# Kernel optimization log

Hardware: AMD Instinct MI355X
Metric: run time of the kernel (lower is better)

Reference implementation:

```python
import jax, jax.numpy as jnp
import numpy as np

NUM_LOW, NUM_HIGH, DIM = 8192, 1024, 2048
EPS = 1e-10


def sparsemax(z):
    # z: [..., K]; Martins & Astudillo sparsemax along last axis.
    K = z.shape[-1]
    z_sorted = jnp.flip(jnp.sort(z, axis=-1), axis=-1)          # descending
    z_cum = jnp.cumsum(z_sorted, axis=-1)
    k = jnp.arange(1, K + 1, dtype=z.dtype)
    support = (1.0 + k * z_sorted) > z_cum                       # bool [..., K]
    k_sup = jnp.sum(support, axis=-1, keepdims=True)             # int [..., 1]
    tau = (jnp.take_along_axis(z_cum, k_sup - 1, axis=-1) - 1.0) / k_sup.astype(z.dtype)
    return jnp.maximum(z - tau, 0.0)


def normalize_rows(x, eps=EPS):
    return x / (jnp.sum(x, axis=1, keepdims=True) + eps)


def setup_inputs() -> dict:
    key = jax.random.key(0)
    k1, k2, k3, k4 = jax.random.split(key, 4)

    def xavier(k, shape):
        bound = float(np.sqrt(6.0 / (shape[0] + shape[1])))
        return jax.random.uniform(k, shape, jnp.float32, -bound, bound)

    return {
        "low_w": xavier(k1, (NUM_LOW, DIM)),    # low Concepts parameter
        "high_w": xavier(k2, (NUM_HIGH, DIM)),  # high Concepts parameter
        "Wq": xavier(k3, (DIM, DIM)),           # q_linear.weight (keep_head_dim, n_head=1)
        "Wk": xavier(k4, (DIM, DIM)),           # k_linear.weight
        "norm_low_concepts": 1,
        "norm_high_concepts": 1,
    }


def reference(low_w, high_w, Wq, Wk, norm_low_concepts, norm_high_concepts):
    # Concepts modules: return (possibly normalized) concepts + cosine similarity.
    low_normed = low_w / jnp.linalg.norm(low_w, axis=1, keepdims=True)
    low_concepts = low_normed if norm_low_concepts else low_w
    low_cos = low_normed @ low_normed.T                          # [NL, NL]

    high_normed = high_w / jnp.linalg.norm(high_w, axis=1, keepdims=True)
    high_concepts = high_normed if norm_high_concepts else high_w
    high_cos = high_normed @ high_normed.T                       # [NH, NH]

    # detach_low_concepts=True -> queries do not receive gradients
    low_q = jax.lax.stop_gradient(low_concepts)

    # ModifiedMultiHeadAttention (n_head=1, keep_head_dim -> d_head=DIM; eval mode,
    # so smooth_max is identity and sparsemax is deterministic).
    q = low_q @ Wq.T                                             # [NL, D]
    k = high_concepts @ Wk.T                                     # [NH, D]
    scale = 1.0 / jnp.sqrt(jnp.asarray(DIM, q.dtype))
    attn = sparsemax((q @ k.T) * scale)                          # [NL, NH]
    high_related_low = attn @ high_concepts                      # [NL, D]

    # output_high_concepts_type == "high_plus_low": add back aggregated low concepts
    aggregated_low = normalize_rows(attn.T) @ low_q              # [NH, D]
    output_high_concepts = high_related_low + attn @ aggregated_low  # [NL, D]

    return (low_concepts, low_cos, output_high_concepts, high_cos, attn)
```

## Files before the change

### kernel.cpp

```cpp
#include <hip/hip_runtime.h>
#include <hip/hip_bf16.h>
#include <stdint.h>

#define NL   8192
#define NHI  1024
#define DIMV 2048

typedef __attribute__((ext_vector_type(8))) short short8;
typedef __attribute__((ext_vector_type(4))) float f32x4;

__device__ __forceinline__ unsigned short f2bf(float x){
  unsigned u = __float_as_uint(x);
  u += 0x7FFFu + ((u >> 16) & 1u);
  return (unsigned short)(u >> 16);
}
__device__ __forceinline__ float bf2f(unsigned short b){
  return __uint_as_float(((unsigned)b) << 16);
}
__device__ __forceinline__ unsigned pack2bf(float a, float b){
  return (unsigned)f2bf(a) | ((unsigned)f2bf(b) << 16);
}

__device__ __forceinline__ void gload16(const void* g, void* l){
  __builtin_amdgcn_global_load_lds(
      (const __attribute__((address_space(1))) unsigned int*)g,
      (__attribute__((address_space(3))) unsigned int*)l, 16, 0, 0);
}

template<int WRITE_F32>
__global__ __launch_bounds__(256)
void rownorm_kernel(const float* __restrict__ W, float* __restrict__ outF32,
                    unsigned short* __restrict__ outBf){
  int row = blockIdx.x;
  const float* r = W + (size_t)row * DIMV;
  int base = threadIdx.x * 8;
  float4 x0 = *(const float4*)(r + base);
  float4 x1 = *(const float4*)(r + base + 4);
  float ss = x0.x*x0.x + x0.y*x0.y + x0.z*x0.z + x0.w*x0.w
           + x1.x*x1.x + x1.y*x1.y + x1.z*x1.z + x1.w*x1.w;
  #pragma unroll
  for(int s = 1; s < 64; s <<= 1) ss += __shfl_xor(ss, s, 64);
  __shared__ float red[4];
  if((threadIdx.x & 63) == 0) red[threadIdx.x >> 6] = ss;
  __syncthreads();
  float tot = red[0] + red[1] + red[2] + red[3];
  float inv = 1.0f / sqrtf(tot);
  float y0=x0.x*inv, y1=x0.y*inv, y2=x0.z*inv, y3=x0.w*inv;
  float y4=x1.x*inv, y5=x1.y*inv, y6=x1.z*inv, y7=x1.w*inv;
  if(WRITE_F32){
    float* o = outF32 + (size_t)row * DIMV + base;
    *(float4*)o       = make_float4(y0,y1,y2,y3);
    *(float4*)(o + 4) = make_float4(y4,y5,y6,y7);
  }
  uint4 u;
  u.x = pack2bf(y0,y1); u.y = pack2bf(y2,y3);
  u.z = pack2bf(y4,y5); u.w = pack2bf(y6,y7);
  *(uint4*)(outBf + (size_t)row * DIMV + base) = u;
}

__global__ __launch_bounds__(256)
void cast_bf16_kernel(const float* __restrict__ in, unsigned short* __restrict__ out){
  size_t i = ((size_t)blockIdx.x * 256 + threadIdx.x) * 8;
  float4 x0 = *(const float4*)(in + i);
  float4 x1 = *(const float4*)(in + i + 4);
  uint4 u;
  u.x = pack2bf(x0.x,x0.y); u.y = pack2bf(x0.z,x0.w);
  u.z = pack2bf(x1.x,x1.y); u.w = pack2bf(x1.z,x1.w);
  *(uint4*)(out + i) = u;
}

template<int OUT_BF16, int MIRROR>
__global__ __launch_bounds__(256, 2)
void gemm_bt_kernel(const unsigned short* __restrict__ A,
                    const unsigned short* __restrict__ Bt,
                    float* __restrict__ Cf, unsigned short* __restrict__ Cb,
                    int M, int N, int K, float scale){
  __shared__ __align__(16) char smem[32768];
  unsigned short* sA = (unsigned short*)smem;
  unsigned short* sB = sA + 128 * 64;

  int tid = threadIdx.x, lane = tid & 63, wid = tid >> 6;
  int mBase, nBase;
  if(MIRROR){
    int nwg = gridDim.x;
    int id = blockIdx.x;
    int cpx = nwg >> 3;
    id = (id & 7) * cpx + (id >> 3);
    int bi = 0;
    while(((bi+1)*64 - (((bi+1)*bi) >> 1)) <= id) bi++;
    int off = bi*64 - ((bi*(bi-1)) >> 1);
    int bj = bi + (id - off);
    mBase = bi * 128; nBase = bj * 128;
  } else {
    int gx = gridDim.x, gy = gridDim.y;
    int nwg = gx * gy;
    int id = blockIdx.y * gx + blockIdx.x;
    if((nwg & 7) == 0){ int cpx = nwg >> 3; id = (id & 7) * cpx + (id >> 3); }
    mBase = (id / gx) * 128; nBase = (id % gx) * 128;
  }

  int chRow = lane >> 3;
  int chCol = (lane & 7) * 8;
  int wm = wid >> 1, wn = wid & 1;

  f32x4 acc[4][4];
  #pragma unroll
  for(int i=0;i<4;i++)
    #pragma unroll
    for(int j=0;j<4;j++) acc[i][j] = (f32x4){0.f,0.f,0.f,0.f};

  int kChunk = K / (int)gridDim.z;
  int kStart = kChunk * (int)blockIdx.z;
  if(!OUT_BF16) Cf += (size_t)blockIdx.z * M * N;

  for(int k0 = kStart; k0 < kStart + kChunk; k0 += 64){
    #pragma unroll
    for(int i = 0; i < 4; i++){
      int ch = wid * 4 + i;
      int arow = ch * 8 + chRow;
      gload16(A  + (size_t)(mBase + arow) * K + k0 + chCol, &sA[ch * 512]);
      gload16(Bt + (size_t)(nBase + arow) * K + k0 + chCol, &sB[ch * 512]);
    }
    __syncthreads();
    #pragma unroll
    for(int kk = 0; kk < 64; kk += 32){
      short8 a[4], b[4];
      int krd = kk + (lane >> 4) * 8;
      #pragma unroll
      for(int i = 0; i < 4; i++){
        int row = wm * 64 + i * 16 + (lane & 15);
        a[i] = *reinterpret_cast<const short8*>(&sA[row * 64 + krd]);
        int col = wn * 64 + i * 16 + (lane & 15);
        b[i] = *reinterpret_cast<const short8*>(&sB[col * 64 + krd]);
      }
      #pragma unroll
      for(int i = 0; i < 4; i++)
        #pragma unroll
        for(int j = 0; j < 4; j++)
          acc[i][j] = __builtin_amdgcn_mfma_f32_16x16x32_bf16(a[i], b[j], acc[i][j], 0, 0, 0);
    }
    __syncthreads();
  }

  #pragma unroll
  for(int i = 0; i < 4; i++){
    #pragma unroll
    for(int j = 0; j < 4; j++){
      int row = mBase + wm * 64 + i * 16 + (lane >> 4) * 4;
      int col = nBase + wn * 64 + j * 16 + (lane & 15);
      #pragma unroll
      for(int r = 0; r < 4; r++){
        float v = acc[i][j][r] * scale;
        size_t off = (size_t)(row + r) * N + col;
        if(OUT_BF16) Cb[off] = f2bf(v);
        else         Cf[off] = v;
      }
    }
  }

  if(MIRROR && mBase != nBase){
    float* tf = (float*)smem;
    #pragma unroll
    for(int rq = 0; rq < 4; rq++){
      int qm = rq >> 1, qn = rq & 1;
      __syncthreads();
      if(wm == qm && wn == qn){
        #pragma unroll
        for(int i = 0; i < 4; i++)
          #pragma unroll
          for(int j = 0; j < 4; j++){
            int rl = i * 16 + (lane >> 4) * 4;
            int cl = j * 16 + (lane & 15);
            #pragma unroll
            for(int r = 0; r < 4; r++)
              tf[(rl + r) * 65 + cl] = acc[i][j][r] * scale;
          }
      }
      __syncthreads();
      int mr = tid >> 2, seg = tid & 3;
      size_t obase = (size_t)(nBase + qn * 64 + mr) * N + mBase + qm * 64 + seg * 16;
      #pragma unroll
      for(int k4 = 0; k4 < 4; k4++){
        float4 v;
        v.x = tf[(seg * 16 + k4 * 4 + 0) * 65 + mr];
        v.y = tf[(seg * 16 + k4 * 4 + 1) * 65 + mr];
        v.z = tf[(seg * 16 + k4 * 4 + 2) * 65 + mr];
        v.w = tf[(seg * 16 + k4 * 4 + 3) * 65 + mr];
        *(float4*)(Cf + obase + k4 * 4) = v;
      }
    }
  }
}

__global__ __launch_bounds__(256)
void sparsemax_kernel(float* __restrict__ S, unsigned short* __restrict__ attnBf){
  int wid = threadIdx.x >> 6, lane = threadIdx.x & 63;
  int row = blockIdx.x * 4 + wid;
  float* z = S + (size_t)row * NHI;
  float v[16];
  #pragma unroll
  for(int j = 0; j < 16; j++) v[j] = z[j * 64 + lane];
  float mx = v[0];
  #pragma unroll
  for(int j = 1; j < 16; j++) mx = fmaxf(mx, v[j]);
  #pragma unroll
  for(int s = 1; s < 64; s <<= 1) mx = fmaxf(mx, __shfl_xor(mx, s, 64));
  float lo = mx - 1.0f, hi = mx;
  for(int it = 0; it < 40; it++){
    float mid = 0.5f * (lo + hi);
    float sum = 0.f;
    #pragma unroll
    for(int j = 0; j < 16; j++) sum += fmaxf(v[j] - mid, 0.f);
    #pragma unroll
    for(int s = 1; s < 64; s <<= 1) sum += __shfl_xor(sum, s, 64);
    if(sum >= 1.0f) lo = mid; else hi = mid;
  }
  float cnt = 0.f, ssum = 0.f;
  #pragma unroll
  for(int j = 0; j < 16; j++){
    if(v[j] > lo){ cnt += 1.f; ssum += v[j]; }
  }
  #pragma unroll
  for(int s = 1; s < 64; s <<= 1){
    cnt  += __shfl_xor(cnt,  s, 64);
    ssum += __shfl_xor(ssum, s, 64);
  }
  float tau = (ssum - 1.0f) / cnt;
  #pragma unroll
  for(int j = 0; j < 16; j++){
    float a = fmaxf(v[j] - tau, 0.f);
    z[j * 64 + lane] = a;
    attnBf[(size_t)row * NHI + j * 64 + lane] = f2bf(a);
  }
}

__global__ __launch_bounds__(256)
void colsum_part_kernel(const float* __restrict__ attn, float* __restrict__ part){
  int chunk = blockIdx.x;
  int t = threadIdx.x;
  const float* p = attn + (size_t)chunk * 32 * NHI;
  float a0=0,a1=0,a2=0,a3=0;
  for(int r = 0; r < 32; r++){
    a0 += p[(size_t)r*NHI + t];
    a1 += p[(size_t)r*NHI + t + 256];
    a2 += p[(size_t)r*NHI + t + 512];
    a3 += p[(size_t)r*NHI + t + 768];
  }
  float* q = part + (size_t)chunk * NHI;
  q[t]=a0; q[t+256]=a1; q[t+512]=a2; q[t+768]=a3;
}
__global__ __launch_bounds__(256)
void colsum_final_kernel(const float* __restrict__ part, float* __restrict__ colsum){
  int c = blockIdx.x * 256 + threadIdx.x;
  float s = 0.f;
  for(int i = 0; i < 256; i++) s += part[(size_t)i * NHI + c];
  colsum[c] = s;
}

__global__ __launch_bounds__(256)
void transpose_bf16_kernel(const unsigned short* __restrict__ in,
                           unsigned short* __restrict__ out, int R, int C){
  __shared__ unsigned short tile[64][65];
  int c0 = blockIdx.x * 64, r0 = blockIdx.y * 64;
  int t = threadIdx.x;
  int ci = t & 63, r4 = t >> 6;
  #pragma unroll
  for(int k = 0; k < 16; k++){
    int r = k * 4 + r4;
    tile[r][ci] = in[(size_t)(r0 + r) * C + c0 + ci];
  }
  __syncthreads();
  #pragma unroll
  for(int k = 0; k < 16; k++){
    int cc = k * 4 + r4;
    out[(size_t)(c0 + cc) * R + r0 + ci] = tile[ci][cc];
  }
}

__global__ __launch_bounds__(256)
void mt_kernel(const unsigned short* __restrict__ highNT, const float* __restrict__ aggP,
               const float* __restrict__ colsum, unsigned short* __restrict__ Mt){
  int idx = blockIdx.x * 256 + threadIdx.x;
  int h = idx & 1023;
  float s = aggP[idx] + aggP[idx + 2097152] + aggP[idx + 4194304] + aggP[idx + 6291456];
  float val = bf2f(highNT[idx]) + s / (colsum[h] + 1e-10f);
  Mt[idx] = f2bf(val);
}

extern "C" void kernel_launch(void* const* d_in, const int* in_sizes, int n_in,
                              void* d_out, int out_size, void* d_ws, size_t ws_size,
                              hipStream_t stream){
  const float* low_w  = (const float*)d_in[0];
  const float* high_w = (const float*)d_in[1];
  const float* Wq     = (const float*)d_in[2];
  const float* Wk     = (const float*)d_in[3];
  float* out = (float*)d_out;

  char* ws = (char*)d_ws;
  unsigned short* lowN  = (unsigned short*)(ws);
  float*          aggP  = (float*)(ws);
  unsigned short* highN = (unsigned short*)(ws + 33554432);
  unsigned short* WqB   = (unsigned short*)(ws + 37748736);
  unsigned short* WkB   = (unsigned short*)(ws + 46137344);
  unsigned short* attnB = (unsigned short*)(ws + 37748736);
  unsigned short* qB    = (unsigned short*)(ws + 54525952);
  unsigned short* lowNT = qB;
  unsigned short* kB    = (unsigned short*)(ws + 88080384);
  float*          part  = (float*)(ws + 88080384);
  float*          colsum= (float*)(ws + 88080384 + 1048576);
  unsigned short* attnT = (unsigned short*)(ws + 92274688);
  unsigned short* Mt    = (unsigned short*)(ws + 109051904);
  unsigned short* highNT= (unsigned short*)(ws + 113246208);

  float* out_lowc    = out;
  float* out_lowcos  = out + 16777216;
  float* out_high    = out + 83886080;
  float* out_highcos = out + 100663296;
  float* out_attn    = out + 101711872;

  const float scl = 1.0f / sqrtf((float)DIMV);

  rownorm_kernel<1><<<NL,  256, 0, stream>>>(low_w,  out_lowc, lowN);
  rownorm_kernel<0><<<NHI, 256, 0, stream>>>(high_w, nullptr,  highN);
  cast_bf16_kernel<<<2048, 256, 0, stream>>>(Wq, WqB);
  cast_bf16_kernel<<<2048, 256, 0, stream>>>(Wk, WkB);
  gemm_bt_kernel<0,1><<<2080, 256, 0, stream>>>(lowN, lowN, out_lowcos, nullptr,
                                                NL, NL, DIMV, 1.0f);
  gemm_bt_kernel<0,0><<<dim3(8,8), 256, 0, stream>>>(highN, highN, out_highcos, nullptr,
                                                     NHI, NHI, DIMV, 1.0f);
  gemm_bt_kernel<1,0><<<dim3(16,64), 256, 0, stream>>>(lowN, WqB, nullptr, qB,
                                                       NL, DIMV, DIMV, 1.0f);
  gemm_bt_kernel<1,0><<<dim3(16,8), 256, 0, stream>>>(highN, WkB, nullptr, kB,
                                                      NHI, DIMV, DIMV, 1.0f);
  gemm_bt_kernel<0,0><<<dim3(8,64), 256, 0, stream>>>(qB, kB, out_attn, nullptr,
                                                      NL, NHI, DIMV, scl);
  sparsemax_kernel<<<NL/4, 256, 0, stream>>>(out_attn, attnB);
  colsum_part_kernel<<<256, 256, 0, stream>>>(out_attn, part);
  colsum_final_kernel<<<4, 256, 0, stream>>>(part, colsum);
  transpose_bf16_kernel<<<dim3(NHI/64, NL/64), 256, 0, stream>>>(attnB, attnT, NL, NHI);
  transpose_bf16_kernel<<<dim3(DIMV/64, NL/64), 256, 0, stream>>>(lowN, lowNT, NL, DIMV);
  transpose_bf16_kernel<<<dim3(DIMV/64, NHI/64), 256, 0, stream>>>(highN, highNT, NHI, DIMV);
  gemm_bt_kernel<0,0><<<dim3(8,16,4), 256, 0, stream>>>(lowNT, attnT, aggP, nullptr,
                                                        DIMV, NHI, NL, 1.0f);
  mt_kernel<<<8192, 256, 0, stream>>>(highNT, aggP, colsum, Mt);
  gemm_bt_kernel<0,0><<<dim3(16,64), 256, 0, stream>>>(attnB, Mt, out_high, nullptr,
                                                       NL, DIMV, NHI, 1.0f);
}
```

Before: 680.8 us.

## Add 256x256-tile 8-wave GEMM with double-buffered async LDS pipeline for large GEMMs

Adds a new GEMM kernel that computes 256x256 output tiles with 512 threads. It double-buffers tiles in LDS through direct global-to-LDS loads with XOR-swizzled columns, and interleaves the next tile's loads with MFMA phases under barriers and raised wave priority. The large GEMMs (low cosine with the mirrored triangle, Q projection, attention scores, final output) move to it, while the smaller ones keep the 128x128 kernel, which loses its mirror path. The larger tiles aim to raise arithmetic intensity and overlap memory with compute. In exchange, the 128KB of LDS limits occupancy, and small grids such as the 128-block score GEMM may underfill the GPU.

```diff
diff --git a/kernel.cpp b/kernel.cpp
--- a/kernel.cpp
+++ b/kernel.cpp
@@ -69,7 +69,167 @@
   *(uint4*)(out + i) = u;
 }
 
+
+__device__ __forceinline__ void stageA2(const unsigned short* __restrict__ G, int ldk,
+                                        int row0, int kt, int scol, char* dst0,
+                                        int tid, int srl){
+  gload16(G + (size_t)(row0 + srl)*ldk + kt*64 + scol, dst0 + tid*16);
+  gload16(G + (size_t)(row0 + 128 + srl)*ldk + kt*64 + scol, dst0 + 16384 + tid*16);
+}
+__device__ __forceinline__ void stageB2(const unsigned short* __restrict__ G, int ldk,
+                                        int row0, int kt, int scol, char* dst0,
+                                        int tid, int srl){
+  gload16(G + (size_t)(row0 + srl)*ldk + kt*64 + scol, dst0 + tid*16);
+  gload16(G + (size_t)(row0 + 64 + srl)*ldk + kt*64 + scol, dst0 + 8192 + tid*16);
+}
+
+#define PHASE(MH, CB, PRE) { \
+  short8 a0_ = *(const short8*)(pa + ((MH)*64 +  0 + rA)*128 + (CB)); \
+  short8 a1_ = *(const short8*)(pa + ((MH)*64 + 16 + rA)*128 + (CB)); \
+  short8 a2_ = *(const short8*)(pa + ((MH)*64 + 32 + rA)*128 + (CB)); \
+  short8 a3_ = *(const short8*)(pa + ((MH)*64 + 48 + rA)*128 + (CB)); \
+  short8 b0_ = *(const short8*)(pb + (rB0 +  0)*128 + (CB)); \
+  short8 b1_ = *(const short8*)(pb + (rB0 + 16)*128 + (CB)); \
+  short8 b2_ = *(const short8*)(pb + (rB0 + 32)*128 + (CB)); \
+  short8 b3_ = *(const short8*)(pb + (rB0 + 48)*128 + (CB)); \
+  PRE; \
+  __builtin_amdgcn_s_barrier(); \
+  asm volatile("s_waitcnt lgkmcnt(0)" ::: "memory"); \
+  __builtin_amdgcn_sched_barrier(0); \
+  __builtin_amdgcn_s_setprio(1); \
+  acc[(MH)*4+0][0] = __builtin_amdgcn_mfma_f32_16x16x32_bf16(a0_, b0_, acc[(MH)*4+0][0],0,0,0); \
+  acc[(MH)*4+0][1] = __builtin_amdgcn_mfma_f32_16x16x32_bf16(a0_, b1_, acc[(MH)*4+0][1],0,0,0); \
+  acc[(MH)*4+0][2] = __builtin_amdgcn_mfma_f32_16x16x32_bf16(a0_, b2_, acc[(MH)*4+0][2],0,0,0); \
+  acc[(MH)*4+0][3] = __builtin_amdgcn_mfma_f32_16x16x32_bf16(a0_, b3_, acc[(MH)*4+0][3],0,0,0); \
+  acc[(MH)*4+1][0] = __builtin_amdgcn_mfma_f32_16x16x32_bf16(a1_, b0_, acc[(MH)*4+1][0],0,0,0); \
+  acc[(MH)*4+1][1] = __builtin_amdgcn_mfma_f32_16x16x32_bf16(a1_, b1_, acc[(MH)*4+1][1],0,0,0); \
+  acc[(MH)*4+1][2] = __builtin_amdgcn_mfma_f32_16x16x32_bf16(a1_, b2_, acc[(MH)*4+1][2],0,0,0); \
+  acc[(MH)*4+1][3] = __builtin_amdgcn_mfma_f32_16x16x32_bf16(a1_, b3_, acc[(MH)*4+1][3],0,0,0); \
+  acc[(MH)*4+2][0] = __builtin_amdgcn_mfma_f32_16x16x32_bf16(a2_, b0_, acc[(MH)*4+2][0],0,0,0); \
+  acc[(MH)*4+2][1] = __builtin_amdgcn_mfma_f32_16x16x32_bf16(a2_, b1_, acc[(MH)*4+2][1],0,0,0); \
+  acc[(MH)*4+2][2] = __builtin_amdgcn_mfma_f32_16x16x32_bf16(a2_, b2_, acc[(MH)*4+2][2],0,0,0); \
+  acc[(MH)*4+2][3] = __builtin_amdgcn_mfma_f32_16x16x32_bf16(a2_, b3_, acc[(MH)*4+2][3],0,0,0); \
+  acc[(MH)*4+3][0] = __builtin_amdgcn_mfma_f32_16x16x32_bf16(a3_, b0_, acc[(MH)*4+3][0],0,0,0); \
+  acc[(MH)*4+3][1] = __builtin_amdgcn_mfma_f32_16x16x32_bf16(a3_, b1_, acc[(MH)*4+3][1],0,0,0); \
+  acc[(MH)*4+3][2] = __builtin_amdgcn_mfma_f32_16x16x32_bf16(a3_, b2_, acc[(MH)*4+3][2],0,0,0); \
+  acc[(MH)*4+3][3] = __builtin_amdgcn_mfma_f32_16x16x32_bf16(a3_, b3_, acc[(MH)*4+3][3],0,0,0); \
+  __builtin_amdgcn_s_setprio(0); \
+  __builtin_amdgcn_s_barrier(); \
+}
+
 template<int OUT_BF16, int MIRROR>
+__global__ __launch_bounds__(512, 2)
+void gemm256_kernel(const unsigned short* __restrict__ A,
+                    const unsigned short* __restrict__ Bt,
+                    float* __restrict__ Cf, unsigned short* __restrict__ Cb,
+                    int M, int N, int K, float scale){
+  __shared__ __align__(16) char smem[131072];
+  int tid = threadIdx.x, lane = tid & 63, wid = tid >> 6;
+  int wm = wid >> 2, wn = wid & 3;
+
+  int mBase, nBase;
+  if(MIRROR){
+    int nwg = gridDim.x;
+    int id = blockIdx.x;
+    int cpx = nwg >> 3;
+    id = (id & 7) * cpx + (id >> 3);
+    int bi = 0;
+    while(((bi+1)*32 - (((bi+1)*bi) >> 1)) <= id) bi++;
+    int off = bi*32 - ((bi*(bi-1)) >> 1);
+    int bj = bi + (id - off);
+    mBase = bi * 256; nBase = bj * 256;
+  } else {
+    int gx = gridDim.x;
+    int nwg = gx * gridDim.y;
+    int id = blockIdx.y * gx + blockIdx.x;
+    if((nwg & 7) == 0){ int cpx = nwg >> 3; id = (id & 7) * cpx + (id >> 3); }
+    mBase = (id / gx) * 256; nBase = (id % gx) * 256;
+  }
+
+  f32x4 acc[8][4];
+  #pragma unroll
+  for(int i=0;i<8;i++)
+    #pragma unroll
+    for(int j=0;j<4;j++) acc[i][j] = (f32x4){0.f,0.f,0.f,0.f};
+
+  int srl  = tid >> 3;
+  int scol = (((tid & 7) * 16) ^ ((srl & 7) << 4)) >> 1;
+  int rA  = lane & 15;
+  int rB0 = (wn & 1) * 64 + rA;
+  int cbK0 = (((lane >> 4) * 16)      ^ ((lane & 7) << 4));
+  int cbK1 = ((64 + (lane >> 4) * 16) ^ ((lane & 7) << 4));
+
+  int nT = K >> 6;
+  stageB2(Bt, K, nBase,       0, scol, smem + 65536,         tid, srl);
+  stageB2(Bt, K, nBase + 128, 0, scol, smem + 65536 + 16384, tid, srl);
+  stageA2(A,  K, mBase,       0, scol, smem,                 tid, srl);
+  stageA2(A,  K, mBase + 64,  0, scol, smem + 8192,          tid, srl);
+  asm volatile("s_waitcnt vmcnt(2)" ::: "memory");
+  __builtin_amdgcn_s_barrier();
+
+  for(int t = 0; t < nT; ++t){
+    int d = t & 1, d1 = d ^ 1, k1 = t + 1;
+    bool st = (k1 < nT);
+    const char* pa = smem + d*32768 + wm*16384;
+    const char* pb = smem + 65536 + d*32768 + (wn>>1)*16384;
+    PHASE(0, cbK0,
+      if(st){ stageB2(Bt, K, nBase, k1, scol, smem + 65536 + d1*32768, tid, srl);
+              asm volatile("s_waitcnt vmcnt(2)" ::: "memory"); }
+      else  { asm volatile("s_waitcnt vmcnt(0)" ::: "memory"); } )
+    PHASE(1, cbK0,
+      if(st) stageB2(Bt, K, nBase + 128, k1, scol, smem + 65536 + d1*32768 + 16384, tid, srl); )
+    PHASE(0, cbK1,
+      if(st) stageA2(A, K, mBase, k1, scol, smem + d1*32768, tid, srl); )
+    PHASE(1, cbK1,
+      if(st){ stageA2(A, K, mBase + 64, k1, scol, smem + d1*32768 + 8192, tid, srl);
+              asm volatile("s_waitcnt vmcnt(2)" ::: "memory"); } )
+  }
+
+  int crow0 = mBase + wm*128 + (lane>>4)*4;
+  int ccol0 = nBase + wn*64 + (lane&15);
+  #pragma unroll
+  for(int i=0;i<8;i++)
+    #pragma unroll
+    for(int j=0;j<4;j++)
+      #pragma unroll
+      for(int r=0;r<4;r++){
+        float v = acc[i][j][r] * scale;
+        size_t off = (size_t)(crow0 + i*16 + r) * N + ccol0 + j*16;
+        if(OUT_BF16) Cb[off] = f2bf(v);
+        else         Cf[off] = v;
+      }
+
+  if(MIRROR && mBase != nBase){
+    float* T = (float*)(void*)(smem + wid * 8448);
+    int ln15 = lane & 15, lh = lane >> 4;
+    #pragma unroll
+    for(int c2 = 0; c2 < 4; c2++){
+      #pragma unroll
+      for(int ii = 0; ii < 2; ii++)
+        #pragma unroll
+        for(int j = 0; j < 4; j++)
+          #pragma unroll
+          for(int r = 0; r < 4; r++)
+            T[(j*16 + ln15)*33 + ii*16 + lh*4 + r] = acc[c2*2+ii][j][r] * scale;
+      asm volatile("s_waitcnt lgkmcnt(0)" ::: "memory");
+      __builtin_amdgcn_sched_barrier(0);
+      size_t gb = (size_t)(nBase + wn*64 + lane) * N + (mBase + wm*128 + c2*32);
+      #pragma unroll
+      for(int k4 = 0; k4 < 8; k4++){
+        float4 v;
+        v.x = T[lane*33 + k4*4 + 0];
+        v.y = T[lane*33 + k4*4 + 1];
+        v.z = T[lane*33 + k4*4 + 2];
+        v.w = T[lane*33 + k4*4 + 3];
+        *(float4*)(Cf + gb + k4*4) = v;
+      }
+      asm volatile("s_waitcnt lgkmcnt(0)" ::: "memory");
+      __builtin_amdgcn_sched_barrier(0);
+    }
+  }
+}
+
+template<int OUT_BF16>
 __global__ __launch_bounds__(256, 2)
 void gemm_bt_kernel(const unsigned short* __restrict__ A,
                     const unsigned short* __restrict__ Bt,
@@ -80,24 +240,11 @@
   unsigned short* sB = sA + 128 * 64;
 
   int tid = threadIdx.x, lane = tid & 63, wid = tid >> 6;
-  int mBase, nBase;
-  if(MIRROR){
-    int nwg = gridDim.x;
-    int id = blockIdx.x;
-    int cpx = nwg >> 3;
-    id = (id & 7) * cpx + (id >> 3);
-    int bi = 0;
-    while(((bi+1)*64 - (((bi+1)*bi) >> 1)) <= id) bi++;
-    int off = bi*64 - ((bi*(bi-1)) >> 1);
-    int bj = bi + (id - off);
-    mBase = bi * 128; nBase = bj * 128;
-  } else {
-    int gx = gridDim.x, gy = gridDim.y;
-    int nwg = gx * gy;
-    int id = blockIdx.y * gx + blockIdx.x;
-    if((nwg & 7) == 0){ int cpx = nwg >> 3; id = (id & 7) * cpx + (id >> 3); }
-    mBase = (id / gx) * 128; nBase = (id % gx) * 128;
-  }
+  int gx = gridDim.x, gy = gridDim.y;
+  int nwg = gx * gy;
+  int id = blockIdx.y * gx + blockIdx.x;
+  if((nwg & 7) == 0){ int cpx = nwg >> 3; id = (id & 7) * cpx + (id >> 3); }
+  int mBase = (id / gx) * 128, nBase = (id % gx) * 128;
 
   int chRow = lane >> 3;
   int chCol = (lane & 7) * 8;
@@ -154,39 +301,6 @@
         size_t off = (size_t)(row + r) * N + col;
         if(OUT_BF16) Cb[off] = f2bf(v);
         else         Cf[off] = v;
-      }
-    }
-  }
-
-  if(MIRROR && mBase != nBase){
-    float* tf = (float*)smem;
-    #pragma unroll
-    for(int rq = 0; rq < 4; rq++){
-      int qm = rq >> 1, qn = rq & 1;
-      __syncthreads();
-      if(wm == qm && wn == qn){
-        #pragma unroll
-        for(int i = 0; i < 4; i++)
-          #pragma unroll
-          for(int j = 0; j < 4; j++){
-            int rl = i * 16 + (lane >> 4) * 4;
-            int cl = j * 16 + (lane & 15);
-            #pragma unroll
-            for(int r = 0; r < 4; r++)
-              tf[(rl + r) * 65 + cl] = acc[i][j][r] * scale;
-          }
-      }
-      __syncthreads();
-      int mr = tid >> 2, seg = tid & 3;
-      size_t obase = (size_t)(nBase + qn * 64 + mr) * N + mBase + qm * 64 + seg * 16;
-      #pragma unroll
-      for(int k4 = 0; k4 < 4; k4++){
-        float4 v;
-        v.x = tf[(seg * 16 + k4 * 4 + 0) * 65 + mr];
-        v.y = tf[(seg * 16 + k4 * 4 + 1) * 65 + mr];
-        v.z = tf[(seg * 16 + k4 * 4 + 2) * 65 + mr];
-        v.w = tf[(seg * 16 + k4 * 4 + 3) * 65 + mr];
-        *(float4*)(Cf + obase + k4 * 4) = v;
       }
     }
   }
@@ -324,15 +438,15 @@
   rownorm_kernel<0><<<NHI, 256, 0, stream>>>(high_w, nullptr,  highN);
   cast_bf16_kernel<<<2048, 256, 0, stream>>>(Wq, WqB);
   cast_bf16_kernel<<<2048, 256, 0, stream>>>(Wk, WkB);
-  gemm_bt_kernel<0,1><<<2080, 256, 0, stream>>>(lowN, lowN, out_lowcos, nullptr,
-                                                NL, NL, DIMV, 1.0f);
-  gemm_bt_kernel<0,0><<<dim3(8,8), 256, 0, stream>>>(highN, highN, out_highcos, nullptr,
-                                                     NHI, NHI, DIMV, 1.0f);
-  gemm_bt_kernel<1,0><<<dim3(16,64), 256, 0, stream>>>(lowN, WqB, nullptr, qB,
-                                                       NL, DIMV, DIMV, 1.0f);
-  gemm_bt_kernel<1,0><<<dim3(16,8), 256, 0, stream>>>(highN, WkB, nullptr, kB,
-                                                      NHI, DIMV, DIMV, 1.0f);
-  gemm_bt_kernel<0,0><<<dim3(8,64), 256, 0, stream>>>(qB, kB, out_attn, nullptr,
+  gemm256_kernel<0,1><<<528, 512, 0, stream>>>(lowN, lowN, out_lowcos, nullptr,
+                                               NL, NL, DIMV, 1.0f);
+  gemm_bt_kernel<0><<<dim3(8,8), 256, 0, stream>>>(highN, highN, out_highcos, nullptr,
+                                                   NHI, NHI, DIMV, 1.0f);
+  gemm256_kernel<1,0><<<dim3(8,32), 512, 0, stream>>>(lowN, WqB, nullptr, qB,
+                                                      NL, DIMV, DIMV, 1.0f);
+  gemm_bt_kernel<1><<<dim3(16,8), 256, 0, stream>>>(highN, WkB, nullptr, kB,
+                                                    NHI, DIMV, DIMV, 1.0f);
+  gemm256_kernel<0,0><<<dim3(4,32), 512, 0, stream>>>(qB, kB, out_attn, nullptr,
                                                       NL, NHI, DIMV, scl);
   sparsemax_kernel<<<NL/4, 256, 0, stream>>>(out_attn, attnB);
   colsum_part_kernel<<<256, 256, 0, stream>>>(out_attn, part);
@@ -340,9 +454,9 @@
   transpose_bf16_kernel<<<dim3(NHI/64, NL/64), 256, 0, stream>>>(attnB, attnT, NL, NHI);
   transpose_bf16_kernel<<<dim3(DIMV/64, NL/64), 256, 0, stream>>>(lowN, lowNT, NL, DIMV);
   transpose_bf16_kernel<<<dim3(DIMV/64, NHI/64), 256, 0, stream>>>(highN, highNT, NHI, DIMV);
-  gemm_bt_kernel<0,0><<<dim3(8,16,4), 256, 0, stream>>>(lowNT, attnT, aggP, nullptr,
-                                                        DIMV, NHI, NL, 1.0f);
+  gemm_bt_kernel<0><<<dim3(8,16,4), 256, 0, stream>>>(lowNT, attnT, aggP, nullptr,
+                                                      DIMV, NHI, NL, 1.0f);
   mt_kernel<<<8192, 256, 0, stream>>>(highNT, aggP, colsum, Mt);
-  gemm_bt_kernel<0,0><<<dim3(16,64), 256, 0, stream>>>(attnB, Mt, out_high, nullptr,
-                                                       NL, DIMV, NHI, 1.0f);
-}
+  gemm256_kernel<0,0><<<dim3(8,32), 512, 0, stream>>>(attnB, Mt, out_high, nullptr,
+                                                      NL, DIMV, NHI, 1.0f);
+}
```

After: 730.2 us. +7.3%, slower.

## Split-K small GEMMs and merge cast and transpose launches

Applied to the files above, without the earlier changes.

The two Wq/Wk casts are merged into one launch, and the three transposes into one kernel with a block-id dispatch. Both are meant to cut launch overhead and the tails of small grids. The high_cos and k-projection GEMMs, which only had 64 and 128 blocks, now use split-K over 2 slices into fp32 scratch plus a combine kernel, to fill more CUs. This adds extra scratch traffic and two small combine launches, and depends on the gemm kernel already handling gridDim.z as a K split and on the scratch regions not overlapping live buffers.

```diff
diff --git a/kernel.cpp b/kernel.cpp
--- a/kernel.cpp
+++ b/kernel.cpp
@@ -59,8 +59,12 @@
 }
 
 __global__ __launch_bounds__(256)
-void cast_bf16_kernel(const float* __restrict__ in, unsigned short* __restrict__ out){
-  size_t i = ((size_t)blockIdx.x * 256 + threadIdx.x) * 8;
+void cast2_kernel(const float* __restrict__ a, const float* __restrict__ b,
+                  unsigned short* __restrict__ oa, unsigned short* __restrict__ ob){
+  int id = blockIdx.x;
+  const float* in; unsigned short* out;
+  if(id < 2048){ in = a; out = oa; } else { in = b; out = ob; id -= 2048; }
+  size_t i = ((size_t)id * 256 + threadIdx.x) * 8;
   float4 x0 = *(const float4*)(in + i);
   float4 x1 = *(const float4*)(in + i + 4);
   uint4 u;
@@ -193,6 +197,31 @@
 }
 
 __global__ __launch_bounds__(256)
+void combine_bf16_kernel(const float* __restrict__ p, unsigned short* __restrict__ out,
+                         size_t stride){
+  size_t i = ((size_t)blockIdx.x * 256 + threadIdx.x) * 8;
+  float4 a0 = *(const float4*)(p + i);
+  float4 a1 = *(const float4*)(p + i + 4);
+  float4 b0 = *(const float4*)(p + stride + i);
+  float4 b1 = *(const float4*)(p + stride + i + 4);
+  uint4 u;
+  u.x = pack2bf(a0.x+b0.x, a0.y+b0.y); u.y = pack2bf(a0.z+b0.z, a0.w+b0.w);
+  u.z = pack2bf(a1.x+b1.x, a1.y+b1.y); u.w = pack2bf(a1.z+b1.z, a1.w+b1.w);
+  *(uint4*)(out + i) = u;
+}
+__global__ __launch_bounds__(256)
+void combine_f32_kernel(const float* __restrict__ p, float* __restrict__ out,
+                        size_t stride){
+  size_t i = ((size_t)blockIdx.x * 256 + threadIdx.x) * 8;
+  float4 a0 = *(const float4*)(p + i);
+  float4 a1 = *(const float4*)(p + i + 4);
+  float4 b0 = *(const float4*)(p + stride + i);
+  float4 b1 = *(const float4*)(p + stride + i + 4);
+  *(float4*)(out + i)     = make_float4(a0.x+b0.x, a0.y+b0.y, a0.z+b0.z, a0.w+b0.w);
+  *(float4*)(out + i + 4) = make_float4(a1.x+b1.x, a1.y+b1.y, a1.z+b1.z, a1.w+b1.w);
+}
+
+__global__ __launch_bounds__(256)
 void sparsemax_kernel(float* __restrict__ S, unsigned short* __restrict__ attnBf){
   int wid = threadIdx.x >> 6, lane = threadIdx.x & 63;
   int row = blockIdx.x * 4 + wid;
@@ -258,10 +287,18 @@
 }
 
 __global__ __launch_bounds__(256)
-void transpose_bf16_kernel(const unsigned short* __restrict__ in,
-                           unsigned short* __restrict__ out, int R, int C){
+void transpose3_kernel(const unsigned short* __restrict__ attnB, unsigned short* __restrict__ attnT,
+                       const unsigned short* __restrict__ lowN,  unsigned short* __restrict__ lowNT,
+                       const unsigned short* __restrict__ highN, unsigned short* __restrict__ highNT){
   __shared__ unsigned short tile[64][65];
-  int c0 = blockIdx.x * 64, r0 = blockIdx.y * 64;
+  int id = blockIdx.x;
+  const unsigned short* in; unsigned short* out; int R, C, tx, ty;
+  if(id < 2048){        in = attnB; out = attnT;  R = NL;  C = NHI;  tx = id & 15; ty = id >> 4; }
+  else if(id < 6144){ id -= 2048;
+                        in = lowN;  out = lowNT;  R = NL;  C = DIMV; tx = id & 31; ty = id >> 5; }
+  else {              id -= 6144;
+                        in = highN; out = highNT; R = NHI; C = DIMV; tx = id & 31; ty = id >> 5; }
+  int c0 = tx * 64, r0 = ty * 64;
   int t = threadIdx.x;
   int ci = t & 63, r4 = t >> 6;
   #pragma unroll
@@ -309,8 +346,10 @@
   float*          part  = (float*)(ws + 88080384);
   float*          colsum= (float*)(ws + 88080384 + 1048576);
   unsigned short* attnT = (unsigned short*)(ws + 92274688);
+  float*          kPart = (float*)(ws + 92274688);
   unsigned short* Mt    = (unsigned short*)(ws + 109051904);
   unsigned short* highNT= (unsigned short*)(ws + 113246208);
+  float*          hcPart= (float*)(ws + 109051904);
 
   float* out_lowc    = out;
   float* out_lowcos  = out + 16777216;
@@ -322,24 +361,23 @@
 
   rownorm_kernel<1><<<NL,  256, 0, stream>>>(low_w,  out_lowc, lowN);
   rownorm_kernel<0><<<NHI, 256, 0, stream>>>(high_w, nullptr,  highN);
-  cast_bf16_kernel<<<2048, 256, 0, stream>>>(Wq, WqB);
-  cast_bf16_kernel<<<2048, 256, 0, stream>>>(Wk, WkB);
+  cast2_kernel<<<4096, 256, 0, stream>>>(Wq, Wk, WqB, WkB);
   gemm_bt_kernel<0,1><<<2080, 256, 0, stream>>>(lowN, lowN, out_lowcos, nullptr,
                                                 NL, NL, DIMV, 1.0f);
-  gemm_bt_kernel<0,0><<<dim3(8,8), 256, 0, stream>>>(highN, highN, out_highcos, nullptr,
-                                                     NHI, NHI, DIMV, 1.0f);
+  gemm_bt_kernel<0,0><<<dim3(8,8,2), 256, 0, stream>>>(highN, highN, hcPart, nullptr,
+                                                       NHI, NHI, DIMV, 1.0f);
+  combine_f32_kernel<<<512, 256, 0, stream>>>(hcPart, out_highcos, 1048576);
   gemm_bt_kernel<1,0><<<dim3(16,64), 256, 0, stream>>>(lowN, WqB, nullptr, qB,
                                                        NL, DIMV, DIMV, 1.0f);
-  gemm_bt_kernel<1,0><<<dim3(16,8), 256, 0, stream>>>(highN, WkB, nullptr, kB,
-                                                      NHI, DIMV, DIMV, 1.0f);
+  gemm_bt_kernel<0,0><<<dim3(16,8,2), 256, 0, stream>>>(highN, WkB, kPart, nullptr,
+                                                        NHI, DIMV, DIMV, 1.0f);
+  combine_bf16_kernel<<<1024, 256, 0, stream>>>(kPart, kB, 2097152);
   gemm_bt_kernel<0,0><<<dim3(8,64), 256, 0, stream>>>(qB, kB, out_attn, nullptr,
                                                       NL, NHI, DIMV, scl);
   sparsemax_kernel<<<NL/4, 256, 0, stream>>>(out_attn, attnB);
   colsum_part_kernel<<<256, 256, 0, stream>>>(out_attn, part);
   colsum_final_kernel<<<4, 256, 0, stream>>>(part, colsum);
-  transpose_bf16_kernel<<<dim3(NHI/64, NL/64), 256, 0, stream>>>(attnB, attnT, NL, NHI);
-  transpose_bf16_kernel<<<dim3(DIMV/64, NL/64), 256, 0, stream>>>(lowN, lowNT, NL, DIMV);
-  transpose_bf16_kernel<<<dim3(DIMV/64, NHI/64), 256, 0, stream>>>(highN, highNT, NHI, DIMV);
+  transpose3_kernel<<<6656, 256, 0, stream>>>(attnB, attnT, lowN, lowNT, highN, highNT);
   gemm_bt_kernel<0,0><<<dim3(8,16,4), 256, 0, stream>>>(lowNT, attnT, aggP, nullptr,
                                                         DIMV, NHI, NL, 1.0f);
   mt_kernel<<<8192, 256, 0, stream>>>(highNT, aggP, colsum, Mt);
```

Result: faster. 642.0 us (-5.7%).
